# Performance work log

Measured on AMD Instinct MI355X. Metric: run time of the kernel, lower is better.

## Reference

```python
import jax, jax.numpy as jnp
import numpy as np

EPS = 0.1           # entropic regularization epsilon
MAX_ITER = 100
THRESH = 0.1        # early-stop threshold on mean |u - u_prev|
LOG_EPS = 1e-8


def setup_inputs() -> dict:
    key = jax.random.key(0)
    kx, ky = jax.random.split(key)
    x = jax.random.normal(kx, (8, 1024, 3), dtype=jnp.float32)
    y = jax.random.normal(ky, (8, 1024, 3), dtype=jnp.float32)
    return {"x": x, "y": y}


def _sqdist(x, y):
    # squared euclidean cost matrix [B, N, N]  (== torch.cdist(x,y,p=2)**2)
    x2 = jnp.sum(x * x, axis=-1)[:, :, None]
    y2 = jnp.sum(y * y, axis=-1)[:, None, :]
    xy = jnp.einsum("bnd,bmd->bnm", x, y)
    return jnp.maximum(x2 + y2 - 2.0 * xy, 0.0)


def reference(x, y):
    B, N, D = x.shape
    C = _sqdist(x, y)                      # [B, N, N]
    log_mu = jnp.log(1.0 / N + LOG_EPS)    # scalar (uniform marginals)
    log_nu = log_mu

    u0 = jnp.zeros((B, N), dtype=x.dtype)
    v0 = jnp.zeros((B, N), dtype=x.dtype)

    def step(carry, _):
        u, v, done = carry
        # u-update uses old v
        M1 = (u[:, :, None] + v[:, None, :] - C) / EPS          # [B,N,N]
        u_new = EPS * (log_mu - jax.nn.logsumexp(M1, axis=-1)) + u
        # v-update uses new u
        M2 = (u_new[:, :, None] + v[:, None, :] - C) / EPS
        v_new = EPS * (log_nu - jax.nn.logsumexp(M2, axis=-2)) + v
        # freeze once converged (mimics torch early break)
        u_out = jnp.where(done, u, u_new)
        v_out = jnp.where(done, v, v_new)
        err = jnp.mean(jnp.abs(u_out - u))
        done_new = done | (err < THRESH)
        return (u_out, v_out, done_new), None

    (u, v, _), _ = jax.lax.scan(step, (u0, v0, jnp.array(False)), None, length=MAX_ITER)

    PI = jnp.exp((u[:, :, None] + v[:, None, :] - C) / EPS)     # transport plan
    emd = jnp.sum(PI * C, axis=(-2, -1))                        # [B]
    return jnp.mean(emd)                                        # reduction='mean'
```

## Files before the change

### kernel.cpp

```cpp
#include <hip/hip_runtime.h>

typedef unsigned int uint_t;
typedef unsigned long long u64_t;

constexpr int B = 8;
constexpr int N = 1024;
constexpr int NBLOCKS = 256;
constexpr int NTHREADS = 512;
constexpr int NWAVES = NTHREADS / 64;
constexpr int BPB = NBLOCKS / B;
constexpr int SEG = N / BPB;
constexpr int RPW = SEG / NWAVES;
constexpr int KPL = N / 64;
constexpr int MAX_ITER = 100;
constexpr float THRESH = 0.1f;
constexpr float K2 = 14.42695040888963f;
constexpr float A2K = 2.0f * K2;
constexpr float NEPSLN2 = -0.06931471805599453f;
constexpr float EPSLOGMU = -0.693146156565634f;
constexpr uint_t MAGIC = 0xC0FFEE01u;

constexpr int OFF_U    = 0;
constexpr int OFF_V    = OFF_U + B * N;
constexpr int OFF_ZERO = OFF_V + B * N;
constexpr int OFF_FLGA = OFF_ZERO;
constexpr int OFF_FLGB = OFF_FLGA + 512;
constexpr int OFF_ERRB = OFF_FLGB + 512;
constexpr int OFF_ZEROEND = OFF_ERRB + 64;
constexpr int OFF_INIT = OFF_ZEROEND;

__device__ __forceinline__ float gload(const float* p) {
  return __hip_atomic_load(p, __ATOMIC_RELAXED, __HIP_MEMORY_SCOPE_AGENT);
}
__device__ __forceinline__ void gstore(float* p, float v) {
  __hip_atomic_store(p, v, __ATOMIC_RELAXED, __HIP_MEMORY_SCOPE_AGENT);
}
__device__ __forceinline__ uint_t l32(const uint_t* p) {
  return __hip_atomic_load(p, __ATOMIC_RELAXED, __HIP_MEMORY_SCOPE_AGENT);
}
__device__ __forceinline__ void s32(uint_t* p, uint_t v) {
  __hip_atomic_store(p, v, __ATOMIC_RELAXED, __HIP_MEMORY_SCOPE_AGENT);
}
__device__ __forceinline__ u64_t l64(const u64_t* p) {
  return __hip_atomic_load(p, __ATOMIC_RELAXED, __HIP_MEMORY_SCOPE_AGENT);
}
__device__ __forceinline__ void s64(u64_t* p, u64_t v) {
  __hip_atomic_store(p, v, __ATOMIC_RELAXED, __HIP_MEMORY_SCOPE_AGENT);
}
__device__ __forceinline__ void drain() { __builtin_amdgcn_s_waitcnt(0); }

__device__ __forceinline__ u64_t pk64(uint_t tag, float v) {
  return ((u64_t)tag << 32) | (u64_t)__float_as_uint(v);
}

__device__ __forceinline__ float wsum(float v) {
#pragma unroll
  for (int o = 32; o; o >>= 1) v += __shfl_xor(v, o);
  return v;
}
__device__ __forceinline__ float wmax(float v) {
#pragma unroll
  for (int o = 32; o; o >>= 1) v = fmaxf(v, __shfl_xor(v, o));
  return v;
}

__device__ __forceinline__ float block_sum(float v, float* sh) {
  v = wsum(v);
  const int wave = threadIdx.x >> 6;
  const int lane = threadIdx.x & 63;
  if (lane == 0) sh[wave] = v;
  __syncthreads();
  float tot = 0.f;
#pragma unroll
  for (int w = 0; w < NWAVES; ++w) tot += sh[w];
  __syncthreads();
  return tot;
}

template <bool TRACK, bool PIN_ZERO>
__device__ __forceinline__ float half_compute(
    const float2* __restrict__ cxy, const float2* __restrict__ czw,
    const float2* __restrict__ rxy, const float2* __restrict__ rzw,
    const float* __restrict__ pin, float* __restrict__ pout,
    const float (&prev)[RPW], float (&pnew)[RPW], int i0, int lane) {
  float p2[KPL];
#pragma unroll
  for (int k = 0; k < KPL; ++k)
    p2[k] = PIN_ZERO ? 0.f : gload(&pin[lane + (k << 6)]) * K2;

  float a0[RPW], a1[RPW], a2[RPW], X[RPW], m[RPW];
  float vals[RPW][KPL];
#pragma unroll
  for (int rr = 0; rr < RPW; ++rr) {
    float2 rA = rxy[i0 + rr], rB = rzw[i0 + rr];
    a0[rr] = A2K * rA.x; a1[rr] = A2K * rA.y; a2[rr] = A2K * rB.x;
    X[rr] = -rB.y;
    m[rr] = -3.4e38f;
  }
#pragma unroll
  for (int k = 0; k < KPL; ++k) {
    const int j = lane + (k << 6);
    float2 cA = cxy[j], cB = czw[j];
    float base = cB.y + p2[k];
#pragma unroll
    for (int rr = 0; rr < RPW; ++rr) {
      float t = fmaf(a0[rr], cA.x, fmaf(a1[rr], cA.y, fmaf(a2[rr], cB.x, base)));
      float val = fminf(t - X[rr], p2[k]);
      vals[rr][k] = val;
      m[rr] = fmaxf(m[rr], val);
    }
  }
  float err = 0.f;
#pragma unroll
  for (int rr = 0; rr < RPW; ++rr) {
    float mr = wmax(m[rr]);
    float s = 0.f;
#pragma unroll
    for (int k = 0; k < KPL; ++k)
      s += __builtin_amdgcn_exp2f(vals[rr][k] - mr);
    s = wsum(s);
    float pn = fmaf(NEPSLN2, mr + __builtin_amdgcn_logf(s), EPSLOGMU);
    pnew[rr] = pn;
    if (lane == 0) {
      gstore(&pout[i0 + rr], pn);
      if (TRACK) err += fabsf(pn - prev[rr]);
    }
  }
  return err;
}

__global__ void __launch_bounds__(NTHREADS, 2) sinkhorn_kernel(
    const float* __restrict__ xg, const float* __restrict__ yg,
    float* __restrict__ out, float* __restrict__ ws) {
  __shared__ float2 s_xxy[N], s_xzw[N];
  __shared__ float2 s_yxy[N], s_yzw[N];
  __shared__ float sh_red[NWAVES];

  const int bid = blockIdx.x;
  const int tid = threadIdx.x;
  const int b = bid & 7;
  const int seg = bid >> 3;
  const int wave = tid >> 6;
  const int lane = tid & 63;
  const int i0 = seg * SEG + wave * RPW;

  float* u = ws + OFF_U + b * N;
  float* v = ws + OFF_V + b * N;
  u64_t* flgA = (u64_t*)(ws + OFF_FLGA) + b * 32;
  u64_t* flgB = (u64_t*)(ws + OFF_FLGB) + b * 32;
  u64_t* flgB_all = (u64_t*)(ws + OFF_FLGB);
  u64_t* errB = (u64_t*)(ws + OFF_ERRB);
  uint_t* init_flag = (uint_t*)(ws + OFF_INIT);

  if (bid == 0) {
    u64_t* zb = (u64_t*)(ws + OFF_ZERO);
    for (int i = tid; i < (OFF_ZEROEND - OFF_ZERO) / 2; i += NTHREADS)
      s64(&zb[i], 0ull);
    drain();
    __syncthreads();
    if (tid == 0) s32(init_flag, MAGIC);
  }

  {
    const float2* xp = (const float2*)(xg + (size_t)b * N * 3) + 3 * tid;
    float2 g0 = xp[0], g1 = xp[1], g2 = xp[2];
    s_xxy[2 * tid]     = g0;
    s_xzw[2 * tid]     = make_float2(g1.x, -K2 * (g0.x * g0.x + g0.y * g0.y + g1.x * g1.x));
    s_xxy[2 * tid + 1] = make_float2(g1.y, g2.x);
    s_xzw[2 * tid + 1] = make_float2(g2.y, -K2 * (g1.y * g1.y + g2.x * g2.x + g2.y * g2.y));
    const float2* yp = (const float2*)(yg + (size_t)b * N * 3) + 3 * tid;
    float2 h0 = yp[0], h1 = yp[1], h2 = yp[2];
    s_yxy[2 * tid]     = h0;
    s_yzw[2 * tid]     = make_float2(h1.x, -K2 * (h0.x * h0.x + h0.y * h0.y + h1.x * h1.x));
    s_yxy[2 * tid + 1] = make_float2(h1.y, h2.x);
    s_yzw[2 * tid + 1] = make_float2(h2.y, -K2 * (h1.y * h1.y + h2.x * h2.x + h2.y * h2.y));
  }
  __syncthreads();

  float un[RPW], un_prev[RPW];
#pragma unroll
  for (int rr = 0; rr < RPW; ++rr) un_prev[rr] = 0.f;
  float my_err = half_compute<true, true>(s_yxy, s_yzw, s_xxy, s_xzw,
                                          v, u, un_prev, un, i0, lane);
  drain();
  float werr = wsum(my_err);
  if (lane == 0) sh_red[wave] = werr;
  if (tid == 0 && bid != 0)
    while (l32(init_flag) != MAGIC) __builtin_amdgcn_s_sleep(2);
  __syncthreads();
  if (tid == 0) {
    float e = 0.f;
#pragma unroll
    for (int w = 0; w < NWAVES; ++w) e += sh_red[w];
    s64(&flgA[seg], pk64(1u, e));
  }

  int it = 0;
  int final_it;
  bool use_prev;
  for (;;) {
    const uint_t want = (uint_t)(it + 1);

    if (wave == 0) {
      float pay;
      for (;;) {
        u64_t pk = (lane < BPB) ? l64(&flgA[lane]) : ~0ull;
        if (__all((uint_t)(pk >> 32) >= want)) { pay = __uint_as_float((uint_t)pk); break; }
        __builtin_amdgcn_s_sleep(1);
      }
      if (seg == 0) {
        float e = wsum((lane < BPB) ? pay : 0.f);
        if (lane == 0) s64(&errB[(it & 3) * 8 + b], pk64(want, e));
      }
    }
    __syncthreads();

    float vn[RPW], vdummy[RPW];
    half_compute<false, false>(s_xxy, s_xzw, s_yxy, s_yzw,
                               u, v, vdummy, vn, i0, lane);
    drain();
    __syncthreads();
    if (tid == 0) s64(&flgB[seg], pk64(want, 0.f));

    if (wave == 0) {
      for (;;) {
        u64_t pk = (lane < BPB) ? l64(&flgB[lane]) : ~0ull;
        if (__all((uint_t)(pk >> 32) >= want)) break;
        __builtin_amdgcn_s_sleep(1);
      }
    }
    __syncthreads();

    if (it == MAX_ITER - 1) { final_it = it + 1; use_prev = false; break; }

    u64_t dpre = (lane < B) ? l64(&errB[(it & 3) * 8 + lane]) : ~0ull;

#pragma unroll
    for (int rr = 0; rr < RPW; ++rr) un_prev[rr] = un[rr];
    my_err = half_compute<true, false>(s_yxy, s_yzw, s_xxy, s_xzw,
                                       v, u, un_prev, un, i0, lane);
    drain();
    werr = wsum(my_err);
    if (lane == 0) sh_red[wave] = werr;
    __syncthreads();
    if (tid == 0) {
      float e = 0.f;
#pragma unroll
      for (int w = 0; w < NWAVES; ++w) e += sh_red[w];
      s64(&flgA[seg], pk64((uint_t)(it + 2), e));
    }

    float tot;
    for (;;) {
      if (__all((uint_t)(dpre >> 32) >= want)) {
        tot = wsum((lane < B) ? __uint_as_float((uint_t)dpre) : 0.f);
        break;
      }
      __builtin_amdgcn_s_sleep(1);
      dpre = (lane < B) ? l64(&errB[(it & 3) * 8 + lane]) : ~0ull;
    }
    if (tot * (1.f / (B * N)) < THRESH) {
      final_it = it + 1; use_prev = true;
      break;
    }
    ++it;
  }

  float p2e[KPL];
#pragma unroll
  for (int k = 0; k < KPL; ++k) p2e[k] = gload(&v[lane + (k << 6)]) * K2;
  float acc = 0.f;
#pragma unroll
  for (int rr = 0; rr < RPW; ++rr) {
    const int i = i0 + rr;
    float2 rA = s_xxy[i], rB = s_xzw[i];
    float a0 = A2K * rA.x, a1 = A2K * rA.y, a2 = A2K * rB.x;
    float X = -rB.y;
    float u2 = (use_prev ? un_prev[rr] : un[rr]) * K2;
#pragma unroll
    for (int k = 0; k < KPL; ++k) {
      const int j = lane + (k << 6);
      float2 cA = s_yxy[j], cB = s_yzw[j];
      float t = fmaf(a0, cA.x, fmaf(a1, cA.y, fmaf(a2, cB.x, cB.y)));
      float kc = fmaxf(X - t, 0.f);
      acc = fmaf(__builtin_amdgcn_exp2f(u2 + p2e[k] - kc), kc, acc);
    }
  }
  float blk = block_sum(acc, sh_red);
  const uint_t ef = (uint_t)(final_it + 1);
  if (tid == 0) s64(&flgB[seg], pk64(ef, blk));

  if (bid == 0) {
    float part = 0.f;
    if (wave < 4) {
      u64_t pk;
      for (;;) {
        pk = l64(&flgB_all[(wave << 6) + lane]);
        if (__all((uint_t)(pk >> 32) >= ef)) break;
        __builtin_amdgcn_s_sleep(1);
      }
      part = __uint_as_float((uint_t)pk);
    }
    float tot = block_sum(part, sh_red);
    if (tid == 0) out[0] = tot * (1.f / (B * K2));
  }
}

extern "C" void kernel_launch(void* const* d_in, const int* in_sizes, int n_in,
                              void* d_out, int out_size, void* d_ws, size_t ws_size,
                              hipStream_t stream) {
  const float* x = (const float*)d_in[0];
  const float* y = (const float*)d_in[1];
  float* out = (float*)d_out;
  float* ws = (float*)d_ws;
  void* args[] = { (void*)&x, (void*)&y, (void*)&out, (void*)&ws };
  hipLaunchCooperativeKernel((const void*)sinkhorn_kernel,
                             dim3(NBLOCKS), dim3(NTHREADS), args, 0, stream);
}
```

Before: 107.5 us.

## Replace block-level flag barriers with tagged double-buffered u/v dataflow polling

Each u/v entry is now stored as a 64-bit word that packs an iteration tag with the value, in double-buffered arrays. Each wave polls the exact data it needs until the tags match, instead of waiting on per-block flags guarded by __syncthreads. The error partials also move to per-wave tagged slots, and the workspace zero-init and magic-flag handshake are removed, which takes block-wide barriers and an extra global round trip off every half-iteration. In exchange, global traffic doubles because values are 64-bit, and there is a risk: without zeroing, stale tags left by a previous launch can match the expected tag, so a reader may consume old data before the current launch has written it.

Result: slower. 113.7 us (+5.7%).

```diff
diff --git a/kernel.cpp b/kernel.cpp
--- a/kernel.cpp
+++ b/kernel.cpp
@@ -18,40 +18,24 @@
 constexpr float A2K = 2.0f * K2;
 constexpr float NEPSLN2 = -0.06931471805599453f;
 constexpr float EPSLOGMU = -0.693146156565634f;
-constexpr uint_t MAGIC = 0xC0FFEE01u;
-
-constexpr int OFF_U    = 0;
-constexpr int OFF_V    = OFF_U + B * N;
-constexpr int OFF_ZERO = OFF_V + B * N;
-constexpr int OFF_FLGA = OFF_ZERO;
-constexpr int OFF_FLGB = OFF_FLGA + 512;
-constexpr int OFF_ERRB = OFF_FLGB + 512;
-constexpr int OFF_ZEROEND = OFF_ERRB + 64;
-constexpr int OFF_INIT = OFF_ZEROEND;
-
-__device__ __forceinline__ float gload(const float* p) {
-  return __hip_atomic_load(p, __ATOMIC_RELAXED, __HIP_MEMORY_SCOPE_AGENT);
-}
-__device__ __forceinline__ void gstore(float* p, float v) {
-  __hip_atomic_store(p, v, __ATOMIC_RELAXED, __HIP_MEMORY_SCOPE_AGENT);
-}
-__device__ __forceinline__ uint_t l32(const uint_t* p) {
-  return __hip_atomic_load(p, __ATOMIC_RELAXED, __HIP_MEMORY_SCOPE_AGENT);
-}
-__device__ __forceinline__ void s32(uint_t* p, uint_t v) {
-  __hip_atomic_store(p, v, __ATOMIC_RELAXED, __HIP_MEMORY_SCOPE_AGENT);
-}
+
+constexpr int Q_U    = 0;
+constexpr int Q_V    = Q_U + 2 * B * N;
+constexpr int Q_ERRA = Q_V + 2 * B * N;
+constexpr int Q_ERRB = Q_ERRA + B * 2 * 256;
+constexpr int Q_EMD  = Q_ERRB + 4 * B;
+
 __device__ __forceinline__ u64_t l64(const u64_t* p) {
   return __hip_atomic_load(p, __ATOMIC_RELAXED, __HIP_MEMORY_SCOPE_AGENT);
 }
 __device__ __forceinline__ void s64(u64_t* p, u64_t v) {
   __hip_atomic_store(p, v, __ATOMIC_RELAXED, __HIP_MEMORY_SCOPE_AGENT);
 }
-__device__ __forceinline__ void drain() { __builtin_amdgcn_s_waitcnt(0); }
-
 __device__ __forceinline__ u64_t pk64(uint_t tag, float v) {
   return ((u64_t)tag << 32) | (u64_t)__float_as_uint(v);
 }
+__device__ __forceinline__ uint_t tg(u64_t v) { return (uint_t)(v >> 32); }
+__device__ __forceinline__ float pay(u64_t v) { return __uint_as_float((uint_t)v); }
 
 __device__ __forceinline__ float wsum(float v) {
 #pragma unroll
@@ -77,16 +61,39 @@
   return tot;
 }
 
+__device__ __forceinline__ void poll16(const u64_t* base, uint_t want, int lane,
+                                       float (&out)[KPL]) {
+  u64_t pk[KPL];
+#pragma unroll
+  for (int k = 0; k < KPL; ++k) pk[k] = l64(&base[lane + (k << 6)]);
+  for (;;) {
+    bool ok = true;
+#pragma unroll
+    for (int k = 0; k < KPL; ++k) ok &= (tg(pk[k]) == want);
+    if (__all(ok)) break;
+    __builtin_amdgcn_s_sleep(1);
+#pragma unroll
+    for (int k = 0; k < KPL; ++k)
+      if (tg(pk[k]) != want) pk[k] = l64(&base[lane + (k << 6)]);
+  }
+#pragma unroll
+  for (int k = 0; k < KPL; ++k) out[k] = pay(pk[k]) * K2;
+}
+
 template <bool TRACK, bool PIN_ZERO>
 __device__ __forceinline__ float half_compute(
     const float2* __restrict__ cxy, const float2* __restrict__ czw,
     const float2* __restrict__ rxy, const float2* __restrict__ rzw,
-    const float* __restrict__ pin, float* __restrict__ pout,
+    const u64_t* __restrict__ pin, u64_t* __restrict__ pout,
+    uint_t tag_in, uint_t tag_out,
     const float (&prev)[RPW], float (&pnew)[RPW], int i0, int lane) {
   float p2[KPL];
-#pragma unroll
-  for (int k = 0; k < KPL; ++k)
-    p2[k] = PIN_ZERO ? 0.f : gload(&pin[lane + (k << 6)]) * K2;
+  if (PIN_ZERO) {
+#pragma unroll
+    for (int k = 0; k < KPL; ++k) p2[k] = 0.f;
+  } else {
+    poll16(pin, tag_in, lane, p2);
+  }
 
   float a0[RPW], a1[RPW], a2[RPW], X[RPW], m[RPW];
   float vals[RPW][KPL];
@@ -122,7 +129,7 @@
     float pn = fmaf(NEPSLN2, mr + __builtin_amdgcn_logf(s), EPSLOGMU);
     pnew[rr] = pn;
     if (lane == 0) {
-      gstore(&pout[i0 + rr], pn);
+      s64(&pout[i0 + rr], pk64(tag_out, pn));
       if (TRACK) err += fabsf(pn - prev[rr]);
     }
   }
@@ -131,11 +138,12 @@
 
 __global__ void __launch_bounds__(NTHREADS, 2) sinkhorn_kernel(
     const float* __restrict__ xg, const float* __restrict__ yg,
-    float* __restrict__ out, float* __restrict__ ws) {
+    float* __restrict__ out, float* __restrict__ wsf) {
   __shared__ float2 s_xxy[N], s_xzw[N];
   __shared__ float2 s_yxy[N], s_yzw[N];
   __shared__ float sh_red[NWAVES];
 
+  u64_t* ws = (u64_t*)wsf;
   const int bid = blockIdx.x;
   const int tid = threadIdx.x;
   const int b = bid & 7;
@@ -144,22 +152,13 @@
   const int lane = tid & 63;
   const int i0 = seg * SEG + wave * RPW;
 
-  float* u = ws + OFF_U + b * N;
-  float* v = ws + OFF_V + b * N;
-  u64_t* flgA = (u64_t*)(ws + OFF_FLGA) + b * 32;
-  u64_t* flgB = (u64_t*)(ws + OFF_FLGB) + b * 32;
-  u64_t* flgB_all = (u64_t*)(ws + OFF_FLGB);
-  u64_t* errB = (u64_t*)(ws + OFF_ERRB);
-  uint_t* init_flag = (uint_t*)(ws + OFF_INIT);
-
-  if (bid == 0) {
-    u64_t* zb = (u64_t*)(ws + OFF_ZERO);
-    for (int i = tid; i < (OFF_ZEROEND - OFF_ZERO) / 2; i += NTHREADS)
-      s64(&zb[i], 0ull);
-    drain();
-    __syncthreads();
-    if (tid == 0) s32(init_flag, MAGIC);
-  }
+  u64_t* u0 = ws + Q_U + (size_t)b * N;
+  u64_t* u1 = ws + Q_U + (size_t)(B + b) * N;
+  u64_t* v0 = ws + Q_V + (size_t)b * N;
+  u64_t* v1 = ws + Q_V + (size_t)(B + b) * N;
+  u64_t* errA = ws + Q_ERRA + (size_t)b * 512;
+  u64_t* errB = ws + Q_ERRB;
+  u64_t* emdF = ws + Q_EMD;
 
   {
     const float2* xp = (const float2*)(xg + (size_t)b * N * 3) + 3 * tid;
@@ -181,18 +180,11 @@
 #pragma unroll
   for (int rr = 0; rr < RPW; ++rr) un_prev[rr] = 0.f;
   float my_err = half_compute<true, true>(s_yxy, s_yzw, s_xxy, s_xzw,
-                                          v, u, un_prev, un, i0, lane);
-  drain();
-  float werr = wsum(my_err);
-  if (lane == 0) sh_red[wave] = werr;
-  if (tid == 0 && bid != 0)
-    while (l32(init_flag) != MAGIC) __builtin_amdgcn_s_sleep(2);
-  __syncthreads();
-  if (tid == 0) {
-    float e = 0.f;
-#pragma unroll
-    for (int w = 0; w < NWAVES; ++w) e += sh_red[w];
-    s64(&flgA[seg], pk64(1u, e));
+                                          nullptr, u1, 0u, 1u,
+                                          un_prev, un, i0, lane);
+  {
+    float we = wsum(my_err);
+    if (lane == 0) s64(&errA[0 * 256 + seg * 8 + wave], pk64(1u, we));
   }
 
   int it = 0;
@@ -200,65 +192,58 @@
   bool use_prev;
   for (;;) {
     const uint_t want = (uint_t)(it + 1);
-
-    if (wave == 0) {
-      float pay;
-      for (;;) {
-        u64_t pk = (lane < BPB) ? l64(&flgA[lane]) : ~0ull;
-        if (__all((uint_t)(pk >> 32) >= want)) { pay = __uint_as_float((uint_t)pk); break; }
-        __builtin_amdgcn_s_sleep(1);
-      }
-      if (seg == 0) {
-        float e = wsum((lane < BPB) ? pay : 0.f);
-        if (lane == 0) s64(&errB[(it & 3) * 8 + b], pk64(want, e));
-      }
-    }
-    __syncthreads();
+    u64_t* ucur = ((it + 1) & 1) ? u1 : u0;
+    u64_t* vcur = ((it + 1) & 1) ? v1 : v0;
 
     float vn[RPW], vdummy[RPW];
     half_compute<false, false>(s_xxy, s_xzw, s_yxy, s_yzw,
-                               u, v, vdummy, vn, i0, lane);
-    drain();
-    __syncthreads();
-    if (tid == 0) s64(&flgB[seg], pk64(want, 0.f));
-
-    if (wave == 0) {
+                               ucur, vcur, want, want, vdummy, vn, i0, lane);
+
+    if (seg == 0 && wave == 0) {
+      const u64_t* ea = errA + (it & 1) * 256;
+      u64_t pa[4];
+#pragma unroll
+      for (int q = 0; q < 4; ++q) pa[q] = l64(&ea[lane + (q << 6)]);
       for (;;) {
-        u64_t pk = (lane < BPB) ? l64(&flgB[lane]) : ~0ull;
-        if (__all((uint_t)(pk >> 32) >= want)) break;
+        bool ok = true;
+#pragma unroll
+        for (int q = 0; q < 4; ++q) ok &= (tg(pa[q]) == want);
+        if (__all(ok)) break;
         __builtin_amdgcn_s_sleep(1);
+#pragma unroll
+        for (int q = 0; q < 4; ++q)
+          if (tg(pa[q]) != want) pa[q] = l64(&ea[lane + (q << 6)]);
       }
-    }
-    __syncthreads();
-
-    if (it == MAX_ITER - 1) { final_it = it + 1; use_prev = false; break; }
-
-    u64_t dpre = (lane < B) ? l64(&errB[(it & 3) * 8 + lane]) : ~0ull;
+      float e = 0.f;
+#pragma unroll
+      for (int q = 0; q < 4; ++q) e += pay(pa[q]);
+      e = wsum(e);
+      if (lane == 0) s64(&errB[(it & 3) * 8 + b], pk64(want, e));
+    }
+
+    if (it == MAX_ITER - 1) { final_it = MAX_ITER; use_prev = false; break; }
+
+    u64_t dp = (lane < B) ? l64(&errB[(it & 3) * 8 + lane]) : 0;
 
 #pragma unroll
     for (int rr = 0; rr < RPW; ++rr) un_prev[rr] = un[rr];
+    u64_t* unxt = ((it + 2) & 1) ? u1 : u0;
     my_err = half_compute<true, false>(s_yxy, s_yzw, s_xxy, s_xzw,
-                                       v, u, un_prev, un, i0, lane);
-    drain();
-    werr = wsum(my_err);
-    if (lane == 0) sh_red[wave] = werr;
-    __syncthreads();
-    if (tid == 0) {
-      float e = 0.f;
-#pragma unroll
-      for (int w = 0; w < NWAVES; ++w) e += sh_red[w];
-      s64(&flgA[seg], pk64((uint_t)(it + 2), e));
-    }
-
-    float tot;
+                                       vcur, unxt, want, (uint_t)(it + 2),
+                                       un_prev, un, i0, lane);
+    {
+      float we = wsum(my_err);
+      if (lane == 0)
+        s64(&errA[((it + 1) & 1) * 256 + seg * 8 + wave], pk64((uint_t)(it + 2), we));
+    }
+
     for (;;) {
-      if (__all((uint_t)(dpre >> 32) >= want)) {
-        tot = wsum((lane < B) ? __uint_as_float((uint_t)dpre) : 0.f);
-        break;
-      }
+      bool ok = (lane >= B) || (tg(dp) == want);
+      if (__all(ok)) break;
       __builtin_amdgcn_s_sleep(1);
-      dpre = (lane < B) ? l64(&errB[(it & 3) * 8 + lane]) : ~0ull;
-    }
+      if (lane < B && tg(dp) != want) dp = l64(&errB[(it & 3) * 8 + lane]);
+    }
+    float tot = wsum((lane < B) ? pay(dp) : 0.f);
     if (tot * (1.f / (B * N)) < THRESH) {
       final_it = it + 1; use_prev = true;
       break;
@@ -266,9 +251,9 @@
     ++it;
   }
 
+  u64_t* vfin = (final_it & 1) ? v1 : v0;
   float p2e[KPL];
-#pragma unroll
-  for (int k = 0; k < KPL; ++k) p2e[k] = gload(&v[lane + (k << 6)]) * K2;
+  poll16(vfin, (uint_t)final_it, lane, p2e);
   float acc = 0.f;
 #pragma unroll
   for (int rr = 0; rr < RPW; ++rr) {
@@ -288,18 +273,18 @@
   }
   float blk = block_sum(acc, sh_red);
   const uint_t ef = (uint_t)(final_it + 1);
-  if (tid == 0) s64(&flgB[seg], pk64(ef, blk));
+  if (tid == 0) s64(&emdF[bid], pk64(ef, blk));
 
   if (bid == 0) {
     float part = 0.f;
     if (wave < 4) {
-      u64_t pk;
+      u64_t pk = l64(&emdF[(wave << 6) + lane]);
       for (;;) {
-        pk = l64(&flgB_all[(wave << 6) + lane]);
-        if (__all((uint_t)(pk >> 32) >= ef)) break;
+        if (__all(tg(pk) == ef)) break;
         __builtin_amdgcn_s_sleep(1);
+        if (tg(pk) != ef) pk = l64(&emdF[(wave << 6) + lane]);
       }
-      part = __uint_as_float((uint_t)pk);
+      part = pay(pk);
     }
     float tot = block_sum(part, sh_red);
     if (tid == 0) out[0] = tot * (1.f / (B * K2));
```
